# Performance work log

Hardware: AMD Instinct MI355X
Metric: run time of the kernel (lower is better)

The kernel has to match this reference:

```python
import jax, jax.numpy as jnp
import numpy as np

N = 100000       # nodes
E = 3200000      # edges (avg degree 32)
IN_F = 256
OUT_F = 128
LRELU_ALPHA = 0.2
EPS = 1e-16


def setup_inputs() -> dict:
    key = jax.random.key(0)
    k1, k2, k3, k4 = jax.random.split(key, 4)
    x = jax.random.normal(k1, (N, IN_F), dtype=jnp.float32)
    edge_index = jax.random.randint(k2, (2, E), 0, N, dtype=jnp.int32)
    # xavier_uniform with gain=calculate_gain('relu')=sqrt(2)
    gain = float(np.sqrt(2.0))
    bw = gain * float(np.sqrt(6.0 / (IN_F + OUT_F)))
    weight = jax.random.uniform(k3, (IN_F, OUT_F), dtype=jnp.float32, minval=-bw, maxval=bw)
    ba = gain * float(np.sqrt(6.0 / (1 + 2 * OUT_F)))
    a = jax.random.uniform(k4, (1, 2 * OUT_F), dtype=jnp.float32, minval=-ba, maxval=ba)
    return {"x": x, "edge_index": edge_index, "weight": weight, "a": a}


def reference(x, edge_index, weight, a):
    src = edge_index[0]
    dst = edge_index[1]
    h = x @ weight                                  # [N, OUT_F]
    # e_edge = a @ cat(h[src], h[dst]) == (h @ a_l)[src] + (h @ a_r)[dst]
    a_l = a[0, :OUT_F]
    a_r = a[0, OUT_F:]
    s_l = h @ a_l                                   # [N]
    s_r = h @ a_r                                   # [N]
    e = s_l[src] + s_r[dst]                         # [E]
    e = jnp.where(e >= 0, e, LRELU_ALPHA * e)       # LeakyReLU
    # segment softmax over src groups
    e_max = jax.ops.segment_max(e, src, num_segments=N)   # [N]
    e_exp = jnp.exp(e - e_max[src])                        # [E]
    denom = jax.ops.segment_sum(e_exp, src, num_segments=N)[src] + EPS
    alpha_e = e_exp / denom                                # [E]
    # out[src] += alpha_e * h[dst]  (sparse A_alpha @ h)
    out = jax.ops.segment_sum(alpha_e[:, None] * h[dst], src, num_segments=N)
    return out
```

## Files before the change

kernel.cpp:

```cpp
#include <hip/hip_runtime.h>

#define GN 100000
#define GE 3200000
#define CAP 128
#define NB 391
#define CHUNK 4096
#define BSTRIDE 9216

typedef __attribute__((ext_vector_type(8))) short bf16x8;
typedef __attribute__((ext_vector_type(4))) float f32x4;

__device__ __forceinline__ unsigned short f2bf(float f) {
    unsigned u = __float_as_uint(f);
    u += 0x7fffu + ((u >> 16) & 1u);
    return (unsigned short)(u >> 16);
}
__device__ __forceinline__ unsigned cvtpk(float lo, float hi) {
    unsigned r;
    asm("v_cvt_pk_bf16_f32 %0, %1, %2" : "=v"(r) : "v"(lo), "v"(hi));
    return r;
}

__global__ __launch_bounds__(256) void wprep_kernel(const float* __restrict__ w,
                                                    unsigned short* __restrict__ wT,
                                                    int* __restrict__ bcursor) {
    if (blockIdx.x >= 32) {
        int j = (blockIdx.x - 32) * 256 + threadIdx.x;
        if (j < NB) bcursor[j] = j * BSTRIDE;
        return;
    }
    int flat4 = blockIdx.x * 256 + threadIdx.x;
    int k  = flat4 >> 5;
    int n4 = (flat4 & 31) * 4;
    float4 v = ((const float4*)w)[flat4];
    wT[(size_t)(n4 + 0) * 256 + k] = f2bf(v.x);
    wT[(size_t)(n4 + 1) * 256 + k] = f2bf(v.y);
    wT[(size_t)(n4 + 2) * 256 + k] = f2bf(v.z);
    wT[(size_t)(n4 + 3) * 256 + k] = f2bf(v.w);
}

__global__ __launch_bounds__(256) void gemm_kernel(const float* __restrict__ x,
                                                   const unsigned short* __restrict__ wT,
                                                   const float* __restrict__ a,
                                                   unsigned short* __restrict__ hq,
                                                   float* __restrict__ s_l,
                                                   float* __restrict__ s_r) {
    __shared__ unsigned short As[2][128][40];
    const int tid  = threadIdx.x;
    const int lane = tid & 63, wid = tid >> 6;
    const int l16  = lane & 15, quad = lane >> 4;
    const int wm   = (wid >> 1) * 64, wn = (wid & 1) * 64;
    const int bm   = blockIdx.x * 128;

    f32x4 acc[4][4] = {};

    const int arow = tid >> 1, ahalf = tid & 1;
    int gr = bm + arow; if (gr >= GN) gr = GN - 1;
    const float* xrow = x + (size_t)gr * 256 + ahalf * 16;

    {
        float4 f0 = *(const float4*)(xrow + 0);
        float4 f1 = *(const float4*)(xrow + 4);
        float4 f2 = *(const float4*)(xrow + 8);
        float4 f3 = *(const float4*)(xrow + 12);
        uint4 u0, u1;
        u0.x = cvtpk(f0.x, f0.y); u0.y = cvtpk(f0.z, f0.w);
        u0.z = cvtpk(f1.x, f1.y); u0.w = cvtpk(f1.z, f1.w);
        u1.x = cvtpk(f2.x, f2.y); u1.y = cvtpk(f2.z, f2.w);
        u1.z = cvtpk(f3.x, f3.y); u1.w = cvtpk(f3.z, f3.w);
        *(uint4*)&As[0][arow][ahalf * 16]     = u0;
        *(uint4*)&As[0][arow][ahalf * 16 + 8] = u1;
    }
    bf16x8 bcur[4];
#pragma unroll
    for (int t = 0; t < 4; ++t)
        bcur[t] = *(const bf16x8*)(wT + (size_t)(wn + t * 16 + l16) * 256 + quad * 8);
    __syncthreads();

#pragma unroll
    for (int ks = 0; ks < 8; ++ks) {
        const int cb = ks & 1;
        bf16x8 bnxt[4];
        uint4 u0, u1;
        if (ks < 7) {
            const int k1 = (ks + 1) * 32;
#pragma unroll
            for (int t = 0; t < 4; ++t)
                bnxt[t] = *(const bf16x8*)(wT + (size_t)(wn + t * 16 + l16) * 256 + k1 + quad * 8);
            float4 f0 = *(const float4*)(xrow + k1);
            float4 f1 = *(const float4*)(xrow + k1 + 4);
            float4 f2 = *(const float4*)(xrow + k1 + 8);
            float4 f3 = *(const float4*)(xrow + k1 + 12);
            u0.x = cvtpk(f0.x, f0.y); u0.y = cvtpk(f0.z, f0.w);
            u0.z = cvtpk(f1.x, f1.y); u0.w = cvtpk(f1.z, f1.w);
            u1.x = cvtpk(f2.x, f2.y); u1.y = cvtpk(f2.z, f2.w);
            u1.z = cvtpk(f3.x, f3.y); u1.w = cvtpk(f3.z, f3.w);
        }
        bf16x8 af[4];
#pragma unroll
        for (int t = 0; t < 4; ++t)
            af[t] = *(const bf16x8*)&As[cb][wm + t * 16 + l16][quad * 8];
#pragma unroll
        for (int ti = 0; ti < 4; ++ti)
#pragma unroll
            for (int tj = 0; tj < 4; ++tj)
                acc[ti][tj] = __builtin_amdgcn_mfma_f32_16x16x32_bf16(af[ti], bcur[tj], acc[ti][tj], 0, 0, 0);
        if (ks < 7) {
            *(uint4*)&As[cb ^ 1][arow][ahalf * 16]     = u0;
            *(uint4*)&As[cb ^ 1][arow][ahalf * 16 + 8] = u1;
            __syncthreads();
#pragma unroll
            for (int t = 0; t < 4; ++t) bcur[t] = bnxt[t];
        }
    }

    float alv[4], arv[4];
#pragma unroll
    for (int tj = 0; tj < 4; ++tj) {
        alv[tj] = a[wn + tj * 16 + l16];
        arv[tj] = a[128 + wn + tj * 16 + l16];
    }
#pragma unroll
    for (int ti = 0; ti < 4; ++ti) {
        float slp[4], srp[4];
#pragma unroll
        for (int r = 0; r < 4; ++r) {
            int row = bm + wm + ti * 16 + quad * 4 + r;
            float v0 = acc[ti][0][r], v1 = acc[ti][1][r], v2 = acc[ti][2][r], v3 = acc[ti][3][r];
            if (row < GN) {
                unsigned short* hp = hq + (size_t)row * 128 + wn + l16;
                hp[0]  = f2bf(v0);
                hp[16] = f2bf(v1);
                hp[32] = f2bf(v2);
                hp[48] = f2bf(v3);
            }
            slp[r] = v0 * alv[0] + v1 * alv[1] + v2 * alv[2] + v3 * alv[3];
            srp[r] = v0 * arv[0] + v1 * arv[1] + v2 * arv[2] + v3 * arv[3];
        }
#pragma unroll
        for (int off = 1; off < 16; off <<= 1)
#pragma unroll
            for (int r = 0; r < 4; ++r) {
                slp[r] += __shfl_xor(slp[r], off, 64);
                srp[r] += __shfl_xor(srp[r], off, 64);
            }
        if (l16 == 0) {
#pragma unroll
            for (int r = 0; r < 4; ++r) {
                int row = bm + wm + ti * 16 + quad * 4 + r;
                if (row < GN) {
                    atomicAdd(&s_l[row], slp[r]);
                    atomicAdd(&s_r[row], srp[r]);
                }
            }
        }
    }
}

__global__ __launch_bounds__(256) void bin_kernel(const int* __restrict__ ei,
                                                  int* __restrict__ bcursor,
                                                  unsigned* __restrict__ binned) {
    __shared__ int h_cnt[NB];
    __shared__ int h_base[NB + 1];
    __shared__ int h_gpos[NB];
    __shared__ int h_cur[NB];
    __shared__ unsigned sbuf[CHUNK];
    __shared__ unsigned short sbkt[CHUNK];
    const int tid = threadIdx.x;
    const int base = blockIdx.x * CHUNK;
    const int cnt = min(CHUNK, GE - base);

    int srcv[CHUNK / 256], dstv[CHUNK / 256];
#pragma unroll
    for (int i = 0; i < CHUNK / 256; ++i) {
        int idx = tid + i * 256;
        if (idx < cnt) { srcv[i] = ei[base + idx]; dstv[i] = ei[GE + base + idx]; }
        else srcv[i] = -1;
    }
    for (int j = tid; j < NB; j += 256) h_cnt[j] = 0;
    __syncthreads();
#pragma unroll
    for (int i = 0; i < CHUNK / 256; ++i)
        if (srcv[i] >= 0) atomicAdd(&h_cnt[srcv[i] >> 8], 1);
    __syncthreads();
    if (tid < 64) {
        int carry = 0;
        for (int b0 = 0; b0 < NB; b0 += 64) {
            int idx = b0 + tid;
            int v = (idx < NB) ? h_cnt[idx] : 0;
            int x = v;
#pragma unroll
            for (int off = 1; off < 64; off <<= 1) {
                int y = __shfl_up(x, off, 64);
                if (tid >= off) x += y;
            }
            if (idx < NB) h_base[idx] = carry + x - v;
            carry += __shfl(x, 63, 64);
        }
        if (tid == 0) h_base[NB] = carry;
    }
    __syncthreads();
    for (int j = tid; j < NB; j += 256) {
        h_cur[j] = h_base[j];
        int c = h_cnt[j];
        if (c) h_gpos[j] = atomicAdd(&bcursor[j], c);
    }
    __syncthreads();
#pragma unroll
    for (int i = 0; i < CHUNK / 256; ++i)
        if (srcv[i] >= 0) {
            int b = srcv[i] >> 8;
            int p = atomicAdd(&h_cur[b], 1);
            sbuf[p] = ((unsigned)(srcv[i] & 255) << 17) | (unsigned)dstv[i];
            sbkt[p] = (unsigned short)b;
        }
    __syncthreads();
    for (int p = tid; p < cnt; p += 256) {
        int b = sbkt[p];
        binned[h_gpos[b] + (p - h_base[b])] = sbuf[p];
    }
}

__global__ __launch_bounds__(1024) void fine_kernel(unsigned* __restrict__ binned,
                                                    const int* __restrict__ bcursor,
                                                    int* __restrict__ rowbeg,
                                                    int* __restrict__ rowend) {
    __shared__ unsigned sedge[BSTRIDE];
    __shared__ int n_cnt[256];
    __shared__ int n_base[256];
    __shared__ int n_cur[256];
    const int b = blockIdx.x;
    const int tid = threadIdx.x;
    const int node0 = b * 256;
    const int nn = min(256, GN - node0);
    const int beg = b * BSTRIDE;
    const int cnt = bcursor[b] - beg;
    if (tid < 256) n_cnt[tid] = 0;
    for (int p = tid; p < cnt; p += 1024) sedge[p] = binned[beg + p];
    __syncthreads();
    for (int p = tid; p < cnt; p += 1024)
        atomicAdd(&n_cnt[sedge[p] >> 17], 1);
    __syncthreads();
    if (tid < 64) {
        int carry = 0;
        for (int b0 = 0; b0 < 256; b0 += 64) {
            int idx = b0 + tid;
            int v = n_cnt[idx];
            int x = v;
#pragma unroll
            for (int off = 1; off < 64; off <<= 1) {
                int y = __shfl_up(x, off, 64);
                if (tid >= off) x += y;
            }
            n_base[idx] = carry + x - v;
            carry += __shfl(x, 63, 64);
        }
    }
    __syncthreads();
    if (tid < nn) {
        rowbeg[node0 + tid] = beg + n_base[tid];
        rowend[node0 + tid] = beg + n_base[tid] + n_cnt[tid];
    }
    if (tid < 256) n_cur[tid] = n_base[tid];
    __syncthreads();
    for (int p = tid; p < cnt; p += 1024) {
        unsigned e = sedge[p];
        int pos = atomicAdd(&n_cur[e >> 17], 1);
        binned[beg + pos] = e & 0x1FFFFu;
    }
}

__global__ __launch_bounds__(256) void aggregate_kernel(const uint4* __restrict__ h4,
                                                        const float* __restrict__ s_l,
                                                        const float* __restrict__ s_r,
                                                        const int* __restrict__ rowbeg,
                                                        const int* __restrict__ rowend,
                                                        const int* __restrict__ adj,
                                                        float* __restrict__ out) {
    __shared__ int   s_dst[4][CAP];
    __shared__ float s_w[4][CAP];
    const int wid = threadIdx.x >> 6, lane = threadIdx.x & 63;
    const int node = blockIdx.x * 4 + wid;
    const int beg = rowbeg[node], end = rowend[node];
    const int deg = end - beg;
    const float sl = s_l[node];

    float m = -1e30f;
    for (int j = lane; j < deg; j += 64) {
        int dst = adj[beg + j];
        float e = sl + s_r[dst];
        e = (e >= 0.f) ? e : 0.2f * e;
        if (j < CAP) { s_dst[wid][j] = dst; s_w[wid][j] = e; }
        m = fmaxf(m, e);
    }
#pragma unroll
    for (int off = 1; off < 64; off <<= 1)
        m = fmaxf(m, __shfl_xor(m, off, 64));
    __syncthreads();

    const int n2 = deg < CAP ? deg : CAP;
    float d = 0.f;
    for (int j = lane; j < n2; j += 64) {
        float w = __expf(s_w[wid][j] - m);
        s_w[wid][j] = w;
        d += w;
    }
    for (int j = CAP + lane; j < deg; j += 64) {
        int dst = adj[beg + j];
        float e = sl + s_r[dst];
        e = (e >= 0.f) ? e : 0.2f * e;
        d += __expf(e - m);
    }
#pragma unroll
    for (int off = 1; off < 64; off <<= 1)
        d += __shfl_xor(d, off, 64);
    const float inv = 1.f / (d + 1e-16f);
    __syncthreads();

    const int fl = lane & 15, grp = lane >> 4;
    f32x4 accA = {0.f, 0.f, 0.f, 0.f}, accB = {0.f, 0.f, 0.f, 0.f};
    int j = 0;
#pragma unroll 2
    for (; j < n2; j += 8) {
        int j0 = j + grp, j1 = j + grp + 4;
        bool a0 = j0 < n2, a1 = j1 < n2;
        int   d0 = s_dst[wid][a0 ? j0 : 0];
        int   d1 = s_dst[wid][a1 ? j1 : 0];
        float w0 = a0 ? s_w[wid][j0] : 0.f;
        float w1 = a1 ? s_w[wid][j1] : 0.f;
        uint4 v0 = h4[(size_t)d0 * 16 + fl];
        uint4 v1 = h4[(size_t)d1 * 16 + fl];
        accA.x += w0 * __uint_as_float(v0.x << 16);
        accA.y += w0 * __uint_as_float(v0.x & 0xffff0000u);
        accA.z += w0 * __uint_as_float(v0.y << 16);
        accA.w += w0 * __uint_as_float(v0.y & 0xffff0000u);
        accB.x += w0 * __uint_as_float(v0.z << 16);
        accB.y += w0 * __uint_as_float(v0.z & 0xffff0000u);
        accB.z += w0 * __uint_as_float(v0.w << 16);
        accB.w += w0 * __uint_as_float(v0.w & 0xffff0000u);
        accA.x += w1 * __uint_as_float(v1.x << 16);
        accA.y += w1 * __uint_as_float(v1.x & 0xffff0000u);
        accA.z += w1 * __uint_as_float(v1.y << 16);
        accA.w += w1 * __uint_as_float(v1.y & 0xffff0000u);
        accB.x += w1 * __uint_as_float(v1.z << 16);
        accB.y += w1 * __uint_as_float(v1.z & 0xffff0000u);
        accB.z += w1 * __uint_as_float(v1.w << 16);
        accB.w += w1 * __uint_as_float(v1.w & 0xffff0000u);
    }
    for (; j < deg; j += 4) {
        int jj = j + grp;
        bool act = jj < deg;
        int dst = act ? adj[beg + jj] : 0;
        float e = sl + s_r[dst];
        e = (e >= 0.f) ? e : 0.2f * e;
        float w = act ? __expf(e - m) : 0.f;
        uint4 v = h4[(size_t)dst * 16 + fl];
        accA.x += w * __uint_as_float(v.x << 16);
        accA.y += w * __uint_as_float(v.x & 0xffff0000u);
        accA.z += w * __uint_as_float(v.y << 16);
        accA.w += w * __uint_as_float(v.y & 0xffff0000u);
        accB.x += w * __uint_as_float(v.z << 16);
        accB.y += w * __uint_as_float(v.z & 0xffff0000u);
        accB.z += w * __uint_as_float(v.w << 16);
        accB.w += w * __uint_as_float(v.w & 0xffff0000u);
    }

#pragma unroll
    for (int off = 16; off < 64; off <<= 1) {
        accA.x += __shfl_xor(accA.x, off, 64);
        accA.y += __shfl_xor(accA.y, off, 64);
        accA.z += __shfl_xor(accA.z, off, 64);
        accA.w += __shfl_xor(accA.w, off, 64);
        accB.x += __shfl_xor(accB.x, off, 64);
        accB.y += __shfl_xor(accB.y, off, 64);
        accB.z += __shfl_xor(accB.z, off, 64);
        accB.w += __shfl_xor(accB.w, off, 64);
    }
    if (lane < 16) {
        float* orow = out + (size_t)node * 128 + fl * 8;
        accA.x *= inv; accA.y *= inv; accA.z *= inv; accA.w *= inv;
        accB.x *= inv; accB.y *= inv; accB.z *= inv; accB.w *= inv;
        *(f32x4*)orow       = accA;
        *(f32x4*)(orow + 4) = accB;
    }
}

extern "C" void kernel_launch(void* const* d_in, const int* in_sizes, int n_in,
                              void* d_out, int out_size, void* d_ws, size_t ws_size,
                              hipStream_t stream) {
    const float* x  = (const float*)d_in[0];
    const int*   ei = (const int*)d_in[1];
    const float* w  = (const float*)d_in[2];
    const float* a  = (const float*)d_in[3];
    float* out = (float*)d_out;

    unsigned short* hq = (unsigned short*)d_ws;
    float* s_l     = (float*)(hq + (size_t)GN * 128);
    float* s_r     = s_l + GN;
    int*   bcursor = (int*)(s_r + GN);
    int*   rowbeg  = bcursor + NB;
    int*   rowend  = rowbeg + GN;
    unsigned* binned = (unsigned*)(rowend + GN);
    unsigned short* wT = (unsigned short*)(binned + (size_t)NB * BSTRIDE);

    hipMemsetAsync(s_l, 0, (size_t)(2 * GN) * sizeof(float), stream);

    wprep_kernel<<<34, 256, 0, stream>>>(w, wT, bcursor);
    gemm_kernel<<<(GN + 127) / 128, 256, 0, stream>>>(x, wT, a, hq, s_l, s_r);
    bin_kernel<<<(GE + CHUNK - 1) / CHUNK, 256, 0, stream>>>(ei, bcursor, binned);
    fine_kernel<<<NB, 1024, 0, stream>>>(binned, bcursor, rowbeg, rowend);
    aggregate_kernel<<<GN / 4, 256, 0, stream>>>((const uint4*)hq, s_l, s_r, rowbeg, rowend,
                                                 (const int*)binned, out);
}
```

Measured before the change: 364.9 us.

## Merge GEMM and edge binning into one interleaved launch; fold memset into prep kernel

Combines the GEMM and the edge-binning kernels into a single launch where even blocks run the GEMM tile and odd blocks bin an edge chunk. The compute-heavy and memory/atomic-heavy work can then overlap on the GPU, and one kernel boundary goes away. The s_l/s_r zeroing moves from hipMemsetAsync into extra blocks of the weight-prep kernel, removing a separate memset launch. The shared-memory union is sized for the larger of the two roles, which may lower occupancy for the GEMM blocks.

```diff
diff --git a/kernel.cpp b/kernel.cpp
--- a/kernel.cpp
+++ b/kernel.cpp
@@ -6,6 +6,7 @@
 #define NB 391
 #define CHUNK 4096
 #define BSTRIDE 9216
+#define GBLK 782
 
 typedef __attribute__((ext_vector_type(8))) short bf16x8;
 typedef __attribute__((ext_vector_type(4))) float f32x4;
@@ -23,201 +24,212 @@
 
 __global__ __launch_bounds__(256) void wprep_kernel(const float* __restrict__ w,
                                                     unsigned short* __restrict__ wT,
-                                                    int* __restrict__ bcursor) {
-    if (blockIdx.x >= 32) {
+                                                    int* __restrict__ bcursor,
+                                                    float* __restrict__ s_l) {
+    if (blockIdx.x < 32) {
+        int flat4 = blockIdx.x * 256 + threadIdx.x;
+        int k  = flat4 >> 5;
+        int n4 = (flat4 & 31) * 4;
+        float4 v = ((const float4*)w)[flat4];
+        wT[(size_t)(n4 + 0) * 256 + k] = f2bf(v.x);
+        wT[(size_t)(n4 + 1) * 256 + k] = f2bf(v.y);
+        wT[(size_t)(n4 + 2) * 256 + k] = f2bf(v.z);
+        wT[(size_t)(n4 + 3) * 256 + k] = f2bf(v.w);
+    } else if (blockIdx.x < 34) {
         int j = (blockIdx.x - 32) * 256 + threadIdx.x;
         if (j < NB) bcursor[j] = j * BSTRIDE;
-        return;
-    }
-    int flat4 = blockIdx.x * 256 + threadIdx.x;
-    int k  = flat4 >> 5;
-    int n4 = (flat4 & 31) * 4;
-    float4 v = ((const float4*)w)[flat4];
-    wT[(size_t)(n4 + 0) * 256 + k] = f2bf(v.x);
-    wT[(size_t)(n4 + 1) * 256 + k] = f2bf(v.y);
-    wT[(size_t)(n4 + 2) * 256 + k] = f2bf(v.z);
-    wT[(size_t)(n4 + 3) * 256 + k] = f2bf(v.w);
-}
-
-__global__ __launch_bounds__(256) void gemm_kernel(const float* __restrict__ x,
-                                                   const unsigned short* __restrict__ wT,
-                                                   const float* __restrict__ a,
-                                                   unsigned short* __restrict__ hq,
-                                                   float* __restrict__ s_l,
-                                                   float* __restrict__ s_r) {
-    __shared__ unsigned short As[2][128][40];
-    const int tid  = threadIdx.x;
-    const int lane = tid & 63, wid = tid >> 6;
-    const int l16  = lane & 15, quad = lane >> 4;
-    const int wm   = (wid >> 1) * 64, wn = (wid & 1) * 64;
-    const int bm   = blockIdx.x * 128;
-
-    f32x4 acc[4][4] = {};
-
-    const int arow = tid >> 1, ahalf = tid & 1;
-    int gr = bm + arow; if (gr >= GN) gr = GN - 1;
-    const float* xrow = x + (size_t)gr * 256 + ahalf * 16;
-
-    {
-        float4 f0 = *(const float4*)(xrow + 0);
-        float4 f1 = *(const float4*)(xrow + 4);
-        float4 f2 = *(const float4*)(xrow + 8);
-        float4 f3 = *(const float4*)(xrow + 12);
-        uint4 u0, u1;
-        u0.x = cvtpk(f0.x, f0.y); u0.y = cvtpk(f0.z, f0.w);
-        u0.z = cvtpk(f1.x, f1.y); u0.w = cvtpk(f1.z, f1.w);
-        u1.x = cvtpk(f2.x, f2.y); u1.y = cvtpk(f2.z, f2.w);
-        u1.z = cvtpk(f3.x, f3.y); u1.w = cvtpk(f3.z, f3.w);
-        *(uint4*)&As[0][arow][ahalf * 16]     = u0;
-        *(uint4*)&As[0][arow][ahalf * 16 + 8] = u1;
-    }
-    bf16x8 bcur[4];
-#pragma unroll
-    for (int t = 0; t < 4; ++t)
-        bcur[t] = *(const bf16x8*)(wT + (size_t)(wn + t * 16 + l16) * 256 + quad * 8);
-    __syncthreads();
-
-#pragma unroll
-    for (int ks = 0; ks < 8; ++ks) {
-        const int cb = ks & 1;
-        bf16x8 bnxt[4];
-        uint4 u0, u1;
-        if (ks < 7) {
-            const int k1 = (ks + 1) * 32;
-#pragma unroll
-            for (int t = 0; t < 4; ++t)
-                bnxt[t] = *(const bf16x8*)(wT + (size_t)(wn + t * 16 + l16) * 256 + k1 + quad * 8);
-            float4 f0 = *(const float4*)(xrow + k1);
-            float4 f1 = *(const float4*)(xrow + k1 + 4);
-            float4 f2 = *(const float4*)(xrow + k1 + 8);
-            float4 f3 = *(const float4*)(xrow + k1 + 12);
+    } else {
+        int i = (blockIdx.x - 34) * 256 + threadIdx.x;
+        if (i < 2 * GN / 4) {
+            float4 z = {0.f, 0.f, 0.f, 0.f};
+            ((float4*)s_l)[i] = z;
+        }
+    }
+}
+
+__global__ __launch_bounds__(256) void gemmbin_kernel(const float* __restrict__ x,
+                                                      const unsigned short* __restrict__ wT,
+                                                      const float* __restrict__ a,
+                                                      unsigned short* __restrict__ hq,
+                                                      float* __restrict__ s_l,
+                                                      float* __restrict__ s_r,
+                                                      const int* __restrict__ ei,
+                                                      int* __restrict__ bcursor,
+                                                      unsigned* __restrict__ binned) {
+    __shared__ __align__(16) char smem[30848];
+    const int half = blockIdx.x >> 1;
+    const int tid = threadIdx.x;
+
+    if ((blockIdx.x & 1) == 0) {
+        unsigned short (*As)[128][40] = (unsigned short (*)[128][40])smem;
+        const int lane = tid & 63, wid = tid >> 6;
+        const int l16  = lane & 15, quad = lane >> 4;
+        const int wm   = (wid >> 1) * 64, wn = (wid & 1) * 64;
+        const int bm   = half * 128;
+
+        f32x4 acc[4][4] = {};
+
+        const int arow = tid >> 1, ahalf = tid & 1;
+        int gr = bm + arow; if (gr >= GN) gr = GN - 1;
+        const float* xrow = x + (size_t)gr * 256 + ahalf * 16;
+
+        {
+            float4 f0 = *(const float4*)(xrow + 0);
+            float4 f1 = *(const float4*)(xrow + 4);
+            float4 f2 = *(const float4*)(xrow + 8);
+            float4 f3 = *(const float4*)(xrow + 12);
+            uint4 u0, u1;
             u0.x = cvtpk(f0.x, f0.y); u0.y = cvtpk(f0.z, f0.w);
             u0.z = cvtpk(f1.x, f1.y); u0.w = cvtpk(f1.z, f1.w);
             u1.x = cvtpk(f2.x, f2.y); u1.y = cvtpk(f2.z, f2.w);
             u1.z = cvtpk(f3.x, f3.y); u1.w = cvtpk(f3.z, f3.w);
-        }
-        bf16x8 af[4];
+            *(uint4*)&As[0][arow][ahalf * 16]     = u0;
+            *(uint4*)&As[0][arow][ahalf * 16 + 8] = u1;
+        }
+        bf16x8 bcur[4];
 #pragma unroll
         for (int t = 0; t < 4; ++t)
-            af[t] = *(const bf16x8*)&As[cb][wm + t * 16 + l16][quad * 8];
-#pragma unroll
-        for (int ti = 0; ti < 4; ++ti)
-#pragma unroll
-            for (int tj = 0; tj < 4; ++tj)
-                acc[ti][tj] = __builtin_amdgcn_mfma_f32_16x16x32_bf16(af[ti], bcur[tj], acc[ti][tj], 0, 0, 0);
-        if (ks < 7) {
-            *(uint4*)&As[cb ^ 1][arow][ahalf * 16]     = u0;
-            *(uint4*)&As[cb ^ 1][arow][ahalf * 16 + 8] = u1;
-            __syncthreads();
-#pragma unroll
-            for (int t = 0; t < 4; ++t) bcur[t] = bnxt[t];
-        }
-    }
-
-    float alv[4], arv[4];
-#pragma unroll
-    for (int tj = 0; tj < 4; ++tj) {
-        alv[tj] = a[wn + tj * 16 + l16];
-        arv[tj] = a[128 + wn + tj * 16 + l16];
-    }
-#pragma unroll
-    for (int ti = 0; ti < 4; ++ti) {
-        float slp[4], srp[4];
-#pragma unroll
-        for (int r = 0; r < 4; ++r) {
-            int row = bm + wm + ti * 16 + quad * 4 + r;
-            float v0 = acc[ti][0][r], v1 = acc[ti][1][r], v2 = acc[ti][2][r], v3 = acc[ti][3][r];
-            if (row < GN) {
-                unsigned short* hp = hq + (size_t)row * 128 + wn + l16;
-                hp[0]  = f2bf(v0);
-                hp[16] = f2bf(v1);
-                hp[32] = f2bf(v2);
-                hp[48] = f2bf(v3);
-            }
-            slp[r] = v0 * alv[0] + v1 * alv[1] + v2 * alv[2] + v3 * alv[3];
-            srp[r] = v0 * arv[0] + v1 * arv[1] + v2 * arv[2] + v3 * arv[3];
-        }
-#pragma unroll
-        for (int off = 1; off < 16; off <<= 1)
-#pragma unroll
-            for (int r = 0; r < 4; ++r) {
-                slp[r] += __shfl_xor(slp[r], off, 64);
-                srp[r] += __shfl_xor(srp[r], off, 64);
-            }
-        if (l16 == 0) {
+            bcur[t] = *(const bf16x8*)(wT + (size_t)(wn + t * 16 + l16) * 256 + quad * 8);
+        __syncthreads();
+
+#pragma unroll
+        for (int ks = 0; ks < 8; ++ks) {
+            const int cb = ks & 1;
+            bf16x8 bnxt[4];
+            uint4 u0, u1;
+            if (ks < 7) {
+                const int k1 = (ks + 1) * 32;
+#pragma unroll
+                for (int t = 0; t < 4; ++t)
+                    bnxt[t] = *(const bf16x8*)(wT + (size_t)(wn + t * 16 + l16) * 256 + k1 + quad * 8);
+                float4 f0 = *(const float4*)(xrow + k1);
+                float4 f1 = *(const float4*)(xrow + k1 + 4);
+                float4 f2 = *(const float4*)(xrow + k1 + 8);
+                float4 f3 = *(const float4*)(xrow + k1 + 12);
+                u0.x = cvtpk(f0.x, f0.y); u0.y = cvtpk(f0.z, f0.w);
+                u0.z = cvtpk(f1.x, f1.y); u0.w = cvtpk(f1.z, f1.w);
+                u1.x = cvtpk(f2.x, f2.y); u1.y = cvtpk(f2.z, f2.w);
+                u1.z = cvtpk(f3.x, f3.y); u1.w = cvtpk(f3.z, f3.w);
+            }
+            bf16x8 af[4];
+#pragma unroll
+            for (int t = 0; t < 4; ++t)
+                af[t] = *(const bf16x8*)&As[cb][wm + t * 16 + l16][quad * 8];
+#pragma unroll
+            for (int ti = 0; ti < 4; ++ti)
+#pragma unroll
+                for (int tj = 0; tj < 4; ++tj)
+                    acc[ti][tj] = __builtin_amdgcn_mfma_f32_16x16x32_bf16(af[ti], bcur[tj], acc[ti][tj], 0, 0, 0);
+            if (ks < 7) {
+                *(uint4*)&As[cb ^ 1][arow][ahalf * 16]     = u0;
+                *(uint4*)&As[cb ^ 1][arow][ahalf * 16 + 8] = u1;
+                __syncthreads();
+#pragma unroll
+                for (int t = 0; t < 4; ++t) bcur[t] = bnxt[t];
+            }
+        }
+
+        float alv[4], arv[4];
+#pragma unroll
+        for (int tj = 0; tj < 4; ++tj) {
+            alv[tj] = a[wn + tj * 16 + l16];
+            arv[tj] = a[128 + wn + tj * 16 + l16];
+        }
+#pragma unroll
+        for (int ti = 0; ti < 4; ++ti) {
+            float slp[4], srp[4];
 #pragma unroll
             for (int r = 0; r < 4; ++r) {
                 int row = bm + wm + ti * 16 + quad * 4 + r;
+                float v0 = acc[ti][0][r], v1 = acc[ti][1][r], v2 = acc[ti][2][r], v3 = acc[ti][3][r];
                 if (row < GN) {
-                    atomicAdd(&s_l[row], slp[r]);
-                    atomicAdd(&s_r[row], srp[r]);
+                    unsigned short* hp = hq + (size_t)row * 128 + wn + l16;
+                    hp[0]  = f2bf(v0);
+                    hp[16] = f2bf(v1);
+                    hp[32] = f2bf(v2);
+                    hp[48] = f2bf(v3);
                 }
-            }
-        }
-    }
-}
-
-__global__ __launch_bounds__(256) void bin_kernel(const int* __restrict__ ei,
-                                                  int* __restrict__ bcursor,
-                                                  unsigned* __restrict__ binned) {
-    __shared__ int h_cnt[NB];
-    __shared__ int h_base[NB + 1];
-    __shared__ int h_gpos[NB];
-    __shared__ int h_cur[NB];
-    __shared__ unsigned sbuf[CHUNK];
-    __shared__ unsigned short sbkt[CHUNK];
-    const int tid = threadIdx.x;
-    const int base = blockIdx.x * CHUNK;
-    const int cnt = min(CHUNK, GE - base);
-
-    int srcv[CHUNK / 256], dstv[CHUNK / 256];
-#pragma unroll
-    for (int i = 0; i < CHUNK / 256; ++i) {
-        int idx = tid + i * 256;
-        if (idx < cnt) { srcv[i] = ei[base + idx]; dstv[i] = ei[GE + base + idx]; }
-        else srcv[i] = -1;
-    }
-    for (int j = tid; j < NB; j += 256) h_cnt[j] = 0;
-    __syncthreads();
-#pragma unroll
-    for (int i = 0; i < CHUNK / 256; ++i)
-        if (srcv[i] >= 0) atomicAdd(&h_cnt[srcv[i] >> 8], 1);
-    __syncthreads();
-    if (tid < 64) {
-        int carry = 0;
-        for (int b0 = 0; b0 < NB; b0 += 64) {
-            int idx = b0 + tid;
-            int v = (idx < NB) ? h_cnt[idx] : 0;
-            int x = v;
-#pragma unroll
-            for (int off = 1; off < 64; off <<= 1) {
-                int y = __shfl_up(x, off, 64);
-                if (tid >= off) x += y;
-            }
-            if (idx < NB) h_base[idx] = carry + x - v;
-            carry += __shfl(x, 63, 64);
-        }
-        if (tid == 0) h_base[NB] = carry;
-    }
-    __syncthreads();
-    for (int j = tid; j < NB; j += 256) {
-        h_cur[j] = h_base[j];
-        int c = h_cnt[j];
-        if (c) h_gpos[j] = atomicAdd(&bcursor[j], c);
-    }
-    __syncthreads();
-#pragma unroll
-    for (int i = 0; i < CHUNK / 256; ++i)
-        if (srcv[i] >= 0) {
-            int b = srcv[i] >> 8;
-            int p = atomicAdd(&h_cur[b], 1);
-            sbuf[p] = ((unsigned)(srcv[i] & 255) << 17) | (unsigned)dstv[i];
-            sbkt[p] = (unsigned short)b;
-        }
-    __syncthreads();
-    for (int p = tid; p < cnt; p += 256) {
-        int b = sbkt[p];
-        binned[h_gpos[b] + (p - h_base[b])] = sbuf[p];
+                slp[r] = v0 * alv[0] + v1 * alv[1] + v2 * alv[2] + v3 * alv[3];
+                srp[r] = v0 * arv[0] + v1 * arv[1] + v2 * arv[2] + v3 * arv[3];
+            }
+#pragma unroll
+            for (int off = 1; off < 16; off <<= 1)
+#pragma unroll
+                for (int r = 0; r < 4; ++r) {
+                    slp[r] += __shfl_xor(slp[r], off, 64);
+                    srp[r] += __shfl_xor(srp[r], off, 64);
+                }
+            if (l16 == 0) {
+#pragma unroll
+                for (int r = 0; r < 4; ++r) {
+                    int row = bm + wm + ti * 16 + quad * 4 + r;
+                    if (row < GN) {
+                        atomicAdd(&s_l[row], slp[r]);
+                        atomicAdd(&s_r[row], srp[r]);
+                    }
+                }
+            }
+        }
+    } else {
+        int* h_cnt  = (int*)smem;
+        int* h_base = h_cnt + NB;
+        int* h_gpos = h_base + NB + 1;
+        int* h_cur  = h_gpos + NB;
+        unsigned* sbuf = (unsigned*)(h_cur + NB);
+        unsigned short* sbkt = (unsigned short*)(sbuf + CHUNK);
+
+        const int base = half * CHUNK;
+        const int cnt = min(CHUNK, GE - base);
+
+        int srcv[CHUNK / 256], dstv[CHUNK / 256];
+#pragma unroll
+        for (int i = 0; i < CHUNK / 256; ++i) {
+            int idx = tid + i * 256;
+            if (idx < cnt) { srcv[i] = ei[base + idx]; dstv[i] = ei[GE + base + idx]; }
+            else srcv[i] = -1;
+        }
+        for (int j = tid; j < NB; j += 256) h_cnt[j] = 0;
+        __syncthreads();
+#pragma unroll
+        for (int i = 0; i < CHUNK / 256; ++i)
+            if (srcv[i] >= 0) atomicAdd(&h_cnt[srcv[i] >> 8], 1);
+        __syncthreads();
+        if (tid < 64) {
+            int carry = 0;
+            for (int b0 = 0; b0 < NB; b0 += 64) {
+                int idx = b0 + tid;
+                int v = (idx < NB) ? h_cnt[idx] : 0;
+                int xx = v;
+#pragma unroll
+                for (int off = 1; off < 64; off <<= 1) {
+                    int y = __shfl_up(xx, off, 64);
+                    if (tid >= off) xx += y;
+                }
+                if (idx < NB) h_base[idx] = carry + xx - v;
+                carry += __shfl(xx, 63, 64);
+            }
+            if (tid == 0) h_base[NB] = carry;
+        }
+        __syncthreads();
+        for (int j = tid; j < NB; j += 256) {
+            h_cur[j] = h_base[j];
+            int c = h_cnt[j];
+            if (c) h_gpos[j] = atomicAdd(&bcursor[j], c);
+        }
+        __syncthreads();
+#pragma unroll
+        for (int i = 0; i < CHUNK / 256; ++i)
+            if (srcv[i] >= 0) {
+                int b = srcv[i] >> 8;
+                int p = atomicAdd(&h_cur[b], 1);
+                sbuf[p] = ((unsigned)(srcv[i] & 255) << 17) | (unsigned)dstv[i];
+                sbkt[p] = (unsigned short)b;
+            }
+        __syncthreads();
+        for (int p = tid; p < cnt; p += 256) {
+            int b = sbkt[p];
+            binned[h_gpos[b] + (p - h_base[b])] = sbuf[p];
+        }
     }
 }
 
@@ -403,11 +415,8 @@
     unsigned* binned = (unsigned*)(rowend + GN);
     unsigned short* wT = (unsigned short*)(binned + (size_t)NB * BSTRIDE);
 
-    hipMemsetAsync(s_l, 0, (size_t)(2 * GN) * sizeof(float), stream);
-
-    wprep_kernel<<<34, 256, 0, stream>>>(w, wT, bcursor);
-    gemm_kernel<<<(GN + 127) / 128, 256, 0, stream>>>(x, wT, a, hq, s_l, s_r);
-    bin_kernel<<<(GE + CHUNK - 1) / CHUNK, 256, 0, stream>>>(ei, bcursor, binned);
+    wprep_kernel<<<34 + (2 * GN / 4 + 255) / 256, 256, 0, stream>>>(w, wT, bcursor, s_l);
+    gemmbin_kernel<<<2 * GBLK, 256, 0, stream>>>(x, wT, a, hq, s_l, s_r, ei, bcursor, binned);
     fine_kernel<<<NB, 1024, 0, stream>>>(binned, bcursor, rowbeg, rowend);
     aggregate_kernel<<<GN / 4, 256, 0, stream>>>((const uint4*)hq, s_l, s_r, rowbeg, rowend,
                                                  (const int*)binned, out);
```

Result: no change. 366.5 us (+0.4%).
